# Optimization experiments

Hardware: AMD Instinct MI355X
Metric: run time of the kernel (lower is better)

## Reference

```python
import jax, jax.numpy as jnp
import numpy as np

TAU = 2.0
NUM_HEADS = 8
EPS = 1e-5
SG_ALPHA = 4.0  # spikingjelly sigmoid surrogate default

@jax.custom_vjp
def spike(x):
    return (x >= 0.0).astype(x.dtype)

def _spike_fwd(x):
    return spike(x), x

def _spike_bwd(x, g):
    sg = jax.nn.sigmoid(SG_ALPHA * x)
    return (g * SG_ALPHA * sg * (1.0 - sg),)

spike.defvjp(_spike_fwd, _spike_bwd)

def lif(x_seq, v_th=1.0):
    # multi-step LIF, hard reset to 0, detach_reset; scan over time dim 0
    def step(v, xt):
        v = v + (xt - v) / TAU
        s = spike(v - v_th)
        v = v * (1.0 - jax.lax.stop_gradient(s))
        return v, s
    _, s = jax.lax.scan(step, jnp.zeros_like(x_seq[0]), x_seq)
    return s

def conv1x1_bn(y, W, b, g, beta, m, var):
    # y: (T,B,C,H,W), W: (Cout,Cin) -- 1x1 conv == channel GEMM; BN in eval mode
    z = jnp.einsum('tbchw,oc->tbohw', y, W)
    if b is not None:
        z = z + b.reshape(1, 1, -1, 1, 1)
    scale = (g * jax.lax.rsqrt(var + EPS)).reshape(1, 1, -1, 1, 1)
    shift = (beta - g * m * jax.lax.rsqrt(var + EPS)).reshape(1, 1, -1, 1, 1)
    return z * scale + shift

def setup_inputs() -> dict:
    key = jax.random.key(0)
    ks = jax.random.split(key, 8)
    T, B, C, H, W = 4, 32, 512, 16, 16
    d = {"x": jax.random.normal(ks[0], (T, B, C, H, W), jnp.float32)}
    d["gate_w"] = jax.random.normal(ks[1], (C, C), jnp.float32) * 0.02
    d["gate_b"] = jnp.zeros((C,), jnp.float32)
    d["q_w"] = jax.random.normal(ks[2], (C, C), jnp.float32) * 0.02
    d["k_w"] = jax.random.normal(ks[3], (C, C), jnp.float32) * 0.02
    d["proj_w"] = jax.random.normal(ks[4], (C, C), jnp.float32) * 0.02
    d["proj_b"] = jnp.zeros((C,), jnp.float32)
    for nm, kk in (("gate", ks[5]), ("q", ks[6]), ("k", ks[7]), ("proj", ks[1])):
        d[nm + "_bn_g"] = jnp.ones((C,), jnp.float32)
        d[nm + "_bn_b"] = jnp.zeros((C,), jnp.float32)
        d[nm + "_bn_m"] = jax.random.normal(kk, (C,), jnp.float32) * 0.1
        d[nm + "_bn_v"] = jnp.ones((C,), jnp.float32)
    return d

def reference(x, gate_w, gate_b, q_w, k_w, proj_w, proj_b,
              gate_bn_g, gate_bn_b, gate_bn_m, gate_bn_v,
              q_bn_g, q_bn_b, q_bn_m, q_bn_v,
              k_bn_g, k_bn_b, k_bn_m, k_bn_v,
              proj_bn_g, proj_bn_b, proj_bn_m, proj_bn_v):
    T, B, C, H, W = x.shape
    N = H * W
    h = NUM_HEADS
    Ch = C // h
    identity = x
    xs = lif(x)  # first_lif
    gate = lif(conv1x1_bn(xs, gate_w, gate_b, gate_bn_g, gate_bn_b, gate_bn_m, gate_bn_v))
    qc = lif(conv1x1_bn(xs, q_w, None, q_bn_g, q_bn_b, q_bn_m, q_bn_v))
    kc = lif(conv1x1_bn(xs, k_w, None, k_bn_g, k_bn_b, k_bn_m, k_bn_v))
    def to_heads(y):
        # (T,B,C,H,W) -> (T,B,heads,N,Ch)
        return y.reshape(T, B, C, N).transpose(0, 1, 3, 2).reshape(T, B, N, h, Ch).transpose(0, 1, 3, 2, 4)
    q = to_heads(qc)
    k = to_heads(kc)
    v = to_heads(kc)  # source bug: x_conv_out undefined; v shares the k pathway
    kv = (k * v).sum(axis=-2, keepdims=True)  # (T,B,h,1,Ch)
    kv = lif(kv, v_th=0.5)  # talking_heads_lif
    a = q * kv  # (T,B,h,N,Ch)
    a = a.transpose(0, 1, 2, 4, 3).reshape(T, B, C, H, W)
    a = a * gate
    out = conv1x1_bn(a, proj_w, proj_b, proj_bn_g, proj_bn_b, proj_bn_m, proj_bn_v) + identity
    return (out, v)
```

## Files before the change

kernel.cpp:

```cpp
#include <hip/hip_runtime.h>
#include <math.h>


typedef __bf16 bf16x8 __attribute__((ext_vector_type(8)));
typedef float f32x4 __attribute__((ext_vector_type(4)));

#define OFF_WB  0u
#define OFF_SS  2097152u
#define OFF_XS  2113536u
#define OFF_GS  35667968u
#define OFF_QS  69222400u
#define OFF_KV  102776832u

__device__ __forceinline__ unsigned short f2bf(float f) {
  unsigned u = __float_as_uint(f);
  u += 0x7fffu + ((u >> 16) & 1u);
  return (unsigned short)(u >> 16);
}

struct PrepParams {
  const float* W[4];
  const float* bias2[2];
  const float* g[4]; const float* be[4]; const float* m[4]; const float* v[4];
};

__global__ __launch_bounds__(256) void prep_kernel(PrepParams p, unsigned char* __restrict__ ws) {
  int w = blockIdx.x, o = blockIdx.y;
  const float* Ws = p.W[w];
  unsigned short* Wb = (unsigned short*)(ws + OFF_WB) + (size_t)w * 262144;
  for (int c = threadIdx.x; c < 512; c += 256)
    Wb[o * 512 + c] = f2bf(Ws[o * 512 + c]);
  if (threadIdx.x == 0) {
    float g = p.g[w][o], be = p.be[w][o], mm = p.m[w][o], vv = p.v[w][o];
    float rs = 1.0f / sqrtf(vv + 1e-5f);
    float scale = g * rs;
    float bias = (w == 0) ? p.bias2[0][o] : ((w == 3) ? p.bias2[1][o] : 0.0f);
    float* ss = (float*)(ws + OFF_SS) + w * 1024;
    ss[o] = scale;
    ss[512 + o] = be - g * mm * rs + scale * bias;
  }
}

__global__ __launch_bounds__(256) void lif1_kernel(const float* __restrict__ x,
                                                   unsigned char* __restrict__ ws) {
  __shared__ unsigned short sp[4][32][65];
  int tid = threadIdx.x;
  int b = blockIdx.z, c0 = blockIdx.y * 32, n0 = blockIdx.x * 64;
  int nl = tid & 63, cb = tid >> 6;
#pragma unroll
  for (int g = 0; g < 8; ++g) {
    int cl = cb + g * 4;
    size_t base = ((size_t)b * 512 + (size_t)(c0 + cl)) * 256 + n0 + nl;
    float v = 0.f;
#pragma unroll
    for (int t = 0; t < 4; ++t) {
      float xv = x[base + (size_t)t * 4194304];
      v += (xv - v) * 0.5f;
      bool s = (v >= 1.f);
      v = s ? 0.f : v;
      sp[t][cl][nl] = s ? 0x3f80 : 0;
    }
  }
  __syncthreads();
  unsigned short* xs = (unsigned short*)(ws + OFF_XS);
#pragma unroll
  for (int it = 0; it < 2; ++it) {
    int s = it * 256 + tid;
    int half = s & 1, n_l = (s >> 1) & 63, t = s >> 7;
    union { unsigned short u[16]; uint4 q[2]; } pk;
#pragma unroll
    for (int j = 0; j < 16; ++j) pk.u[j] = sp[t][half * 16 + j][n_l];
    size_t off = ((size_t)(t * 32 + b) * 256 + (size_t)(n0 + n_l)) * 512 + c0 + half * 16;
    *(uint4*)(xs + off) = pk.q[0];
    *(uint4*)(xs + off + 8) = pk.q[1];
  }
}

__global__ __launch_bounds__(256, 2) void gemm3_kernel(unsigned char* __restrict__ ws,
                                                       float* __restrict__ vout) {
  __shared__ __align__(16) unsigned short lA[128 * 72];
  __shared__ __align__(16) unsigned short lB[64 * 72];
  __shared__ unsigned short lT[128 * 65];
  int tid = threadIdx.x;
  int w = blockIdx.z >> 5, b = blockIdx.z & 31;
  int o0 = blockIdx.y * 128, n0 = blockIdx.x * 64;
  int lane = tid & 63, wid = tid >> 6;
  int wm = (wid >> 1) * 64, wn = (wid & 1) * 32;
  const unsigned short* Wb = (const unsigned short*)(ws + OFF_WB) + (size_t)w * 262144;
  const unsigned short* xs = (const unsigned short*)(ws + OFF_XS);
  const float* ss = (const float*)(ws + OFF_SS) + w * 1024;
  unsigned short* spout = (w == 0) ? (unsigned short*)(ws + OFF_GS)
                                   : (unsigned short*)(ws + OFF_QS);

  float vstate[4][2][4];
#pragma unroll
  for (int mf = 0; mf < 4; ++mf)
#pragma unroll
    for (int nf = 0; nf < 2; ++nf)
#pragma unroll
      for (int r = 0; r < 4; ++r) vstate[mf][nf][r] = 0.f;

  for (int t = 0; t < 4; ++t) {
    f32x4 acc[4][2];
#pragma unroll
    for (int mf = 0; mf < 4; ++mf)
#pragma unroll
      for (int nf = 0; nf < 2; ++nf) acc[mf][nf] = (f32x4){0.f, 0.f, 0.f, 0.f};
    const unsigned short* xrow = xs + ((size_t)(t * 32 + b) * 256 + n0) * 512;

    for (int ks = 0; ks < 8; ++ks) {
      __syncthreads();
#pragma unroll
      for (int i = 0; i < 4; ++i) {
        int s = i * 256 + tid;
        int r = s >> 3, kc = (s & 7) * 8;
        *(uint4*)&lA[r * 72 + kc] =
            *(const uint4*)(Wb + (size_t)(o0 + r) * 512 + ks * 64 + kc);
      }
#pragma unroll
      for (int i = 0; i < 2; ++i) {
        int s = i * 256 + tid;
        int r = s >> 3, kc = (s & 7) * 8;
        *(uint4*)&lB[r * 72 + kc] =
            *(const uint4*)(xrow + (size_t)r * 512 + ks * 64 + kc);
      }
      __syncthreads();
#pragma unroll
      for (int ksub = 0; ksub < 2; ++ksub) {
        int kof = ksub * 32 + (lane >> 4) * 8;
        bf16x8 af[4], bfr[2];
#pragma unroll
        for (int mf = 0; mf < 4; ++mf)
          af[mf] = *(const bf16x8*)&lA[(wm + mf * 16 + (lane & 15)) * 72 + kof];
#pragma unroll
        for (int nf = 0; nf < 2; ++nf)
          bfr[nf] = *(const bf16x8*)&lB[(wn + nf * 16 + (lane & 15)) * 72 + kof];
#pragma unroll
        for (int mf = 0; mf < 4; ++mf)
#pragma unroll
          for (int nf = 0; nf < 2; ++nf)
            acc[mf][nf] = __builtin_amdgcn_mfma_f32_16x16x32_bf16(
                af[mf], bfr[nf], acc[mf][nf], 0, 0, 0);
      }
    }
    __syncthreads();
#pragma unroll
    for (int mf = 0; mf < 4; ++mf)
#pragma unroll
      for (int nf = 0; nf < 2; ++nf)
#pragma unroll
        for (int r = 0; r < 4; ++r) {
          int ol = wm + mf * 16 + (lane >> 4) * 4 + r;
          int nn = wn + nf * 16 + (lane & 15);
          int o = o0 + ol;
          float val = acc[mf][nf][r] * ss[o] + ss[512 + o];
          float vs = vstate[mf][nf][r];
          vs += (val - vs) * 0.5f;
          bool s = (vs >= 1.f);
          vstate[mf][nf][r] = s ? 0.f : vs;
          lT[ol * 65 + nn] = s ? 0x3f80 : 0;
        }
    __syncthreads();
    if (w < 2) {
#pragma unroll
      for (int it = 0; it < 2; ++it) {
        int s = it * 256 + tid;
        int n_l = s >> 3, oc = (s & 7) * 16;
        union { unsigned short u[16]; uint4 q[2]; } pk;
#pragma unroll
        for (int j = 0; j < 16; ++j) pk.u[j] = lT[(oc + j) * 65 + n_l];
        size_t off = ((size_t)(t * 32 + b) * 256 + (size_t)(n0 + n_l)) * 512 + o0 + oc;
        *(uint4*)(spout + off) = pk.q[0];
        *(uint4*)(spout + off + 8) = pk.q[1];
      }
    } else {
#pragma unroll
      for (int it = 0; it < 4; ++it) {
        int s = it * 256 + tid;
        int n_l = s >> 4, oc = (s & 15) * 8;
        int o = o0 + oc;
        int h = o >> 6, ch = o & 63;
        float4 f0, f1;
        f0.x = lT[(oc + 0) * 65 + n_l] ? 1.f : 0.f;
        f0.y = lT[(oc + 1) * 65 + n_l] ? 1.f : 0.f;
        f0.z = lT[(oc + 2) * 65 + n_l] ? 1.f : 0.f;
        f0.w = lT[(oc + 3) * 65 + n_l] ? 1.f : 0.f;
        f1.x = lT[(oc + 4) * 65 + n_l] ? 1.f : 0.f;
        f1.y = lT[(oc + 5) * 65 + n_l] ? 1.f : 0.f;
        f1.z = lT[(oc + 6) * 65 + n_l] ? 1.f : 0.f;
        f1.w = lT[(oc + 7) * 65 + n_l] ? 1.f : 0.f;
        size_t off = (((size_t)(t * 32 + b) * 8 + h) * 256 + (size_t)(n0 + n_l)) * 64 + ch;
        *(float4*)(vout + off) = f0;
        *(float4*)(vout + off + 4) = f1;
      }
    }
  }
}

__global__ __launch_bounds__(256) void kv_kernel(const float* __restrict__ vout,
                                                 unsigned char* __restrict__ ws) {
  __shared__ float red[4][64];
  int tid = threadIdx.x;
  int b = blockIdx.x >> 3, hb = blockIdx.x & 7;
  int ch = tid & 63, ng = tid >> 6;
  unsigned short* kvs = (unsigned short*)(ws + OFF_KV);
  float vm = 0.f;
  for (int t = 0; t < 4; ++t) {
    size_t base = (((size_t)(t * 32 + b) * 8 + hb) * 256 + (size_t)ng * 64) * 64 + ch;
    float sum = 0.f;
#pragma unroll 8
    for (int i = 0; i < 64; ++i) sum += vout[base + (size_t)i * 64];
    red[ng][ch] = sum;
    __syncthreads();
    if (ng == 0) {
      float tot = red[0][ch] + red[1][ch] + red[2][ch] + red[3][ch];
      vm += (tot - vm) * 0.5f;
      bool s = (vm >= 0.5f);
      vm = s ? 0.f : vm;
      kvs[(size_t)(t * 32 + b) * 512 + hb * 64 + ch] = s ? 0x3f80 : 0;
    }
    __syncthreads();
  }
}

__global__ __launch_bounds__(256, 2) void proj_kernel(const unsigned char* __restrict__ ws,
                                                      const float* __restrict__ x,
                                                      float* __restrict__ out) {
  __shared__ __align__(16) unsigned short lA[128 * 72];
  __shared__ __align__(16) unsigned short lB[128 * 72];
  int tid = threadIdx.x;
  int t = blockIdx.z >> 5, b = blockIdx.z & 31;
  int o0 = blockIdx.y * 128, n0 = blockIdx.x * 128;
  int lane = tid & 63, wid = tid >> 6;
  int wm = (wid >> 1) * 64, wn = (wid & 1) * 64;
  const unsigned short* Wb = (const unsigned short*)(ws + OFF_WB) + (size_t)3 * 262144;
  const unsigned short* qs =
      (const unsigned short*)(ws + OFF_QS) + ((size_t)(t * 32 + b) * 256 + n0) * 512;
  const unsigned short* gs =
      (const unsigned short*)(ws + OFF_GS) + ((size_t)(t * 32 + b) * 256 + n0) * 512;
  const unsigned short* kvp =
      (const unsigned short*)(ws + OFF_KV) + (size_t)(t * 32 + b) * 512;
  const float* ss = (const float*)(ws + OFF_SS) + 3 * 1024;

  f32x4 acc[4][4];
#pragma unroll
  for (int mf = 0; mf < 4; ++mf)
#pragma unroll
    for (int nf = 0; nf < 4; ++nf) acc[mf][nf] = (f32x4){0.f, 0.f, 0.f, 0.f};

  for (int ks = 0; ks < 8; ++ks) {
    __syncthreads();
#pragma unroll
    for (int i = 0; i < 4; ++i) {
      int s = i * 256 + tid;
      int r = s >> 3, kc = (s & 7) * 8;
      *(uint4*)&lA[r * 72 + kc] =
          *(const uint4*)(Wb + (size_t)(o0 + r) * 512 + ks * 64 + kc);
    }
#pragma unroll
    for (int i = 0; i < 4; ++i) {
      int s = i * 256 + tid;
      int r = s >> 3, kc = (s & 7) * 8;
      size_t e = (size_t)r * 512 + ks * 64 + kc;
      uint4 qv = *(const uint4*)(qs + e);
      uint4 gv = *(const uint4*)(gs + e);
      uint4 kvv = *(const uint4*)(kvp + ks * 64 + kc);
      uint4 av;
      av.x = qv.x & gv.x & kvv.x;
      av.y = qv.y & gv.y & kvv.y;
      av.z = qv.z & gv.z & kvv.z;
      av.w = qv.w & gv.w & kvv.w;
      *(uint4*)&lB[r * 72 + kc] = av;
    }
    __syncthreads();
#pragma unroll
    for (int ksub = 0; ksub < 2; ++ksub) {
      int kof = ksub * 32 + (lane >> 4) * 8;
      bf16x8 af[4], bfr[4];
#pragma unroll
      for (int mf = 0; mf < 4; ++mf)
        af[mf] = *(const bf16x8*)&lA[(wm + mf * 16 + (lane & 15)) * 72 + kof];
#pragma unroll
      for (int nf = 0; nf < 4; ++nf)
        bfr[nf] = *(const bf16x8*)&lB[(wn + nf * 16 + (lane & 15)) * 72 + kof];
#pragma unroll
      for (int mf = 0; mf < 4; ++mf)
#pragma unroll
        for (int nf = 0; nf < 4; ++nf)
          acc[mf][nf] = __builtin_amdgcn_mfma_f32_16x16x32_bf16(
              af[mf], bfr[nf], acc[mf][nf], 0, 0, 0);
    }
  }
#pragma unroll
  for (int mf = 0; mf < 4; ++mf)
#pragma unroll
    for (int r = 0; r < 4; ++r) {
      int o = o0 + wm + mf * 16 + (lane >> 4) * 4 + r;
      float scale = ss[o], shift = ss[512 + o];
#pragma unroll
      for (int nf = 0; nf < 4; ++nf) {
        int nn = n0 + wn + nf * 16 + (lane & 15);
        size_t idx = ((size_t)(t * 32 + b) * 512 + o) * 256 + nn;
        out[idx] = acc[mf][nf][r] * scale + shift + x[idx];
      }
    }
}

extern "C" void kernel_launch(void* const* d_in, const int* in_sizes, int n_in,
                              void* d_out, int out_size, void* d_ws, size_t ws_size,
                              hipStream_t stream) {
  const float* x = (const float*)d_in[0];
  unsigned char* ws = (unsigned char*)d_ws;
  float* out = (float*)d_out;
  float* vout = out + 16777216;

  PrepParams p;
  p.W[0] = (const float*)d_in[1];
  p.W[1] = (const float*)d_in[3];
  p.W[2] = (const float*)d_in[4];
  p.W[3] = (const float*)d_in[5];
  p.bias2[0] = (const float*)d_in[2];
  p.bias2[1] = (const float*)d_in[6];
  const int bni[4] = {7, 11, 15, 19};
  for (int w = 0; w < 4; ++w) {
    p.g[w]  = (const float*)d_in[bni[w] + 0];
    p.be[w] = (const float*)d_in[bni[w] + 1];
    p.m[w]  = (const float*)d_in[bni[w] + 2];
    p.v[w]  = (const float*)d_in[bni[w] + 3];
  }

  prep_kernel<<<dim3(4, 512), dim3(256), 0, stream>>>(p, ws);
  lif1_kernel<<<dim3(4, 16, 32), dim3(256), 0, stream>>>(x, ws);
  gemm3_kernel<<<dim3(4, 4, 96), dim3(256), 0, stream>>>(ws, vout);
  kv_kernel<<<dim3(256), dim3(256), 0, stream>>>(vout, ws);
  proj_kernel<<<dim3(2, 4, 128), dim3(256), 0, stream>>>(ws, x, out);
}
```

Measured before the change: 397.3 us.

## Use direct global-to-LDS loads with XOR swizzle and fuse kv reduction into gemm3

The GEMM tile loads for the weight and spike operands now go straight from global memory into LDS via global_load_lds, with an XOR-swizzled unpadded layout so the fragment reads stay free of bank conflicts. This removes the register round-trip and the padding. The k-pathway spike counts per channel are now reduced inside gemm3's epilogue into a small partial-sum buffer. kv_kernel therefore no longer rereads the full fp32 v output and only combines four partials per channel. Occupancy hints rise to 3 blocks per CU, which may pressure registers.

```diff
diff --git a/kernel.cpp b/kernel.cpp
--- a/kernel.cpp
+++ b/kernel.cpp
@@ -5,17 +5,24 @@
 typedef __bf16 bf16x8 __attribute__((ext_vector_type(8)));
 typedef float f32x4 __attribute__((ext_vector_type(4)));
 
-#define OFF_WB  0u
-#define OFF_SS  2097152u
-#define OFF_XS  2113536u
-#define OFF_GS  35667968u
-#define OFF_QS  69222400u
-#define OFF_KV  102776832u
+#define OFF_WB    0u
+#define OFF_SS    2097152u
+#define OFF_XS    2113536u
+#define OFF_GS    35667968u
+#define OFF_QS    69222400u
+#define OFF_KV    102776832u
+#define OFF_KVACC 102907904u
 
 __device__ __forceinline__ unsigned short f2bf(float f) {
   unsigned u = __float_as_uint(f);
   u += 0x7fffu + ((u >> 16) & 1u);
   return (unsigned short)(u >> 16);
+}
+
+__device__ __forceinline__ void gload16(const void* g, void* l) {
+  __builtin_amdgcn_global_load_lds(
+      (const __attribute__((address_space(1))) void*)g,
+      (__attribute__((address_space(3))) void*)l, 16, 0, 0);
 }
 
 struct PrepParams {
@@ -76,16 +83,21 @@
   }
 }
 
-__global__ __launch_bounds__(256, 2) void gemm3_kernel(unsigned char* __restrict__ ws,
-                                                       float* __restrict__ vout) {
-  __shared__ __align__(16) unsigned short lA[128 * 72];
-  __shared__ __align__(16) unsigned short lB[64 * 72];
+__global__ __launch_bounds__(256, 3) void gemm3_kernel(unsigned char* __restrict__ ws,
+                                                       float* __restrict__ vout,
+                                                       float* __restrict__ kvacc) {
+  __shared__ __align__(16) unsigned short lA[128 * 64];
+  __shared__ __align__(16) unsigned short lB[64 * 64];
   __shared__ unsigned short lT[128 * 65];
   int tid = threadIdx.x;
   int w = blockIdx.z >> 5, b = blockIdx.z & 31;
   int o0 = blockIdx.y * 128, n0 = blockIdx.x * 64;
   int lane = tid & 63, wid = tid >> 6;
   int wm = (wid >> 1) * 64, wn = (wid & 1) * 32;
+  int l8 = lane >> 3, l7 = lane & 7;
+  int swzk = (l7 ^ l8) << 3;
+  int fr = lane & 15, fhi = lane >> 4;
+  int swzf = (lane & 7) << 3;
   const unsigned short* Wb = (const unsigned short*)(ws + OFF_WB) + (size_t)w * 262144;
   const unsigned short* xs = (const unsigned short*)(ws + OFF_XS);
   const float* ss = (const float*)(ws + OFF_SS) + w * 1024;
@@ -112,29 +124,25 @@
       __syncthreads();
 #pragma unroll
       for (int i = 0; i < 4; ++i) {
-        int s = i * 256 + tid;
-        int r = s >> 3, kc = (s & 7) * 8;
-        *(uint4*)&lA[r * 72 + kc] =
-            *(const uint4*)(Wb + (size_t)(o0 + r) * 512 + ks * 64 + kc);
+        int r = wid * 32 + i * 8 + l8;
+        gload16(Wb + (size_t)(o0 + r) * 512 + ks * 64 + swzk, lA + wid * 2048 + i * 512);
       }
 #pragma unroll
       for (int i = 0; i < 2; ++i) {
-        int s = i * 256 + tid;
-        int r = s >> 3, kc = (s & 7) * 8;
-        *(uint4*)&lB[r * 72 + kc] =
-            *(const uint4*)(xrow + (size_t)r * 512 + ks * 64 + kc);
+        int r = wid * 16 + i * 8 + l8;
+        gload16(xrow + (size_t)r * 512 + ks * 64 + swzk, lB + wid * 1024 + i * 512);
       }
       __syncthreads();
 #pragma unroll
       for (int ksub = 0; ksub < 2; ++ksub) {
-        int kof = ksub * 32 + (lane >> 4) * 8;
+        int kof = (ksub * 32 + fhi * 8) ^ swzf;
         bf16x8 af[4], bfr[2];
 #pragma unroll
         for (int mf = 0; mf < 4; ++mf)
-          af[mf] = *(const bf16x8*)&lA[(wm + mf * 16 + (lane & 15)) * 72 + kof];
+          af[mf] = *(const bf16x8*)&lA[(wm + mf * 16 + fr) * 64 + kof];
 #pragma unroll
         for (int nf = 0; nf < 2; ++nf)
-          bfr[nf] = *(const bf16x8*)&lB[(wn + nf * 16 + (lane & 15)) * 72 + kof];
+          bfr[nf] = *(const bf16x8*)&lB[(wn + nf * 16 + fr) * 64 + kof];
 #pragma unroll
         for (int mf = 0; mf < 4; ++mf)
 #pragma unroll
@@ -193,46 +201,53 @@
         *(float4*)(vout + off) = f0;
         *(float4*)(vout + off + 4) = f1;
       }
-    }
-  }
-}
-
-__global__ __launch_bounds__(256) void kv_kernel(const float* __restrict__ vout,
+      {
+        int o = tid >> 1, nh = (tid & 1) * 32;
+        int cnt = 0;
+#pragma unroll
+        for (int n = 0; n < 32; ++n) cnt += (lT[o * 65 + nh + n] ? 1 : 0);
+        cnt += __shfl_xor(cnt, 1);
+        if ((tid & 1) == 0)
+          kvacc[((size_t)(t * 32 + b) * 4 + blockIdx.x) * 512 + o0 + o] = (float)cnt;
+      }
+    }
+  }
+}
+
+__global__ __launch_bounds__(256) void kv_kernel(const float* __restrict__ kvacc,
                                                  unsigned char* __restrict__ ws) {
-  __shared__ float red[4][64];
-  int tid = threadIdx.x;
-  int b = blockIdx.x >> 3, hb = blockIdx.x & 7;
-  int ch = tid & 63, ng = tid >> 6;
+  int b = blockIdx.x;
   unsigned short* kvs = (unsigned short*)(ws + OFF_KV);
-  float vm = 0.f;
-  for (int t = 0; t < 4; ++t) {
-    size_t base = (((size_t)(t * 32 + b) * 8 + hb) * 256 + (size_t)ng * 64) * 64 + ch;
-    float sum = 0.f;
-#pragma unroll 8
-    for (int i = 0; i < 64; ++i) sum += vout[base + (size_t)i * 64];
-    red[ng][ch] = sum;
-    __syncthreads();
-    if (ng == 0) {
-      float tot = red[0][ch] + red[1][ch] + red[2][ch] + red[3][ch];
+#pragma unroll
+  for (int j = 0; j < 2; ++j) {
+    int c = j * 256 + threadIdx.x;
+    float vm = 0.f;
+#pragma unroll
+    for (int t = 0; t < 4; ++t) {
+      const float* p = kvacc + (size_t)(t * 32 + b) * 2048 + c;
+      float tot = p[0] + p[512] + p[1024] + p[1536];
       vm += (tot - vm) * 0.5f;
       bool s = (vm >= 0.5f);
       vm = s ? 0.f : vm;
-      kvs[(size_t)(t * 32 + b) * 512 + hb * 64 + ch] = s ? 0x3f80 : 0;
-    }
-    __syncthreads();
-  }
-}
-
-__global__ __launch_bounds__(256, 2) void proj_kernel(const unsigned char* __restrict__ ws,
+      kvs[(size_t)(t * 32 + b) * 512 + c] = s ? 0x3f80 : 0;
+    }
+  }
+}
+
+__global__ __launch_bounds__(256, 3) void proj_kernel(const unsigned char* __restrict__ ws,
                                                       const float* __restrict__ x,
                                                       float* __restrict__ out) {
-  __shared__ __align__(16) unsigned short lA[128 * 72];
+  __shared__ __align__(16) unsigned short lA[128 * 64];
   __shared__ __align__(16) unsigned short lB[128 * 72];
   int tid = threadIdx.x;
   int t = blockIdx.z >> 5, b = blockIdx.z & 31;
   int o0 = blockIdx.y * 128, n0 = blockIdx.x * 128;
   int lane = tid & 63, wid = tid >> 6;
   int wm = (wid >> 1) * 64, wn = (wid & 1) * 64;
+  int l8 = lane >> 3, l7 = lane & 7;
+  int swzk = (l7 ^ l8) << 3;
+  int fr = lane & 15, fhi = lane >> 4;
+  int swzf = (lane & 7) << 3;
   const unsigned short* Wb = (const unsigned short*)(ws + OFF_WB) + (size_t)3 * 262144;
   const unsigned short* qs =
       (const unsigned short*)(ws + OFF_QS) + ((size_t)(t * 32 + b) * 256 + n0) * 512;
@@ -252,10 +267,8 @@
     __syncthreads();
 #pragma unroll
     for (int i = 0; i < 4; ++i) {
-      int s = i * 256 + tid;
-      int r = s >> 3, kc = (s & 7) * 8;
-      *(uint4*)&lA[r * 72 + kc] =
-          *(const uint4*)(Wb + (size_t)(o0 + r) * 512 + ks * 64 + kc);
+      int r = wid * 32 + i * 8 + l8;
+      gload16(Wb + (size_t)(o0 + r) * 512 + ks * 64 + swzk, lA + wid * 2048 + i * 512);
     }
 #pragma unroll
     for (int i = 0; i < 4; ++i) {
@@ -275,14 +288,15 @@
     __syncthreads();
 #pragma unroll
     for (int ksub = 0; ksub < 2; ++ksub) {
-      int kof = ksub * 32 + (lane >> 4) * 8;
+      int kofA = (ksub * 32 + fhi * 8) ^ swzf;
+      int kofB = ksub * 32 + fhi * 8;
       bf16x8 af[4], bfr[4];
 #pragma unroll
       for (int mf = 0; mf < 4; ++mf)
-        af[mf] = *(const bf16x8*)&lA[(wm + mf * 16 + (lane & 15)) * 72 + kof];
+        af[mf] = *(const bf16x8*)&lA[(wm + mf * 16 + fr) * 64 + kofA];
 #pragma unroll
       for (int nf = 0; nf < 4; ++nf)
-        bfr[nf] = *(const bf16x8*)&lB[(wn + nf * 16 + (lane & 15)) * 72 + kof];
+        bfr[nf] = *(const bf16x8*)&lB[(wn + nf * 16 + fr) * 72 + kofB];
 #pragma unroll
       for (int mf = 0; mf < 4; ++mf)
 #pragma unroll
@@ -313,6 +327,7 @@
   unsigned char* ws = (unsigned char*)d_ws;
   float* out = (float*)d_out;
   float* vout = out + 16777216;
+  float* kvacc = (float*)(ws + OFF_KVACC);
 
   PrepParams p;
   p.W[0] = (const float*)d_in[1];
@@ -331,7 +346,7 @@
 
   prep_kernel<<<dim3(4, 512), dim3(256), 0, stream>>>(p, ws);
   lif1_kernel<<<dim3(4, 16, 32), dim3(256), 0, stream>>>(x, ws);
-  gemm3_kernel<<<dim3(4, 4, 96), dim3(256), 0, stream>>>(ws, vout);
-  kv_kernel<<<dim3(256), dim3(256), 0, stream>>>(vout, ws);
+  gemm3_kernel<<<dim3(4, 4, 96), dim3(256), 0, stream>>>(ws, vout, kvacc);
+  kv_kernel<<<dim3(32), dim3(256), 0, stream>>>(kvacc, ws);
   proj_kernel<<<dim3(2, 4, 128), dim3(256), 0, stream>>>(ws, x, out);
 }
```

Result: faster. 370.0 us (-6.9%).
